# Kernel optimization log

Measured on AMD Instinct MI355X. Metric: run time of the kernel, lower is better.

The kernel has to match this reference:

```python
import jax, jax.numpy as jnp
import numpy as np

N = 100000
E = 1250000
D = 64
R = 16


def _glorot(key, shape):
    fan_in, fan_out = shape[-2], shape[-1]
    lim = jnp.sqrt(6.0 / (fan_in + fan_out))
    return jax.random.uniform(key, shape, jnp.float32, -lim, lim)


def setup_inputs() -> dict:
    key = jax.random.key(0)
    ks = jax.random.split(key, 9)
    x = jax.random.normal(ks[0], (N, D), jnp.float32)
    edge_index = jax.random.randint(ks[1], (2, E), 0, N, jnp.int64 if jax.config.jax_enable_x64 else jnp.int32).astype(jnp.int32)
    edge_type = jax.random.randint(ks[2], (E,), 0, R).astype(jnp.int32)
    return {
        "x": x,
        "edge_index": edge_index,
        "edge_type": edge_type,
        "W1": _glorot(ks[3], (R, D, D)),
        "sw1": _glorot(ks[4], (D, D)),
        "b1": jnp.zeros((D,), jnp.float32),
        "W2": _glorot(ks[5], (R, D, D)),
        "sw2": _glorot(ks[6], (D, D)),
        "b2": jnp.zeros((D,), jnp.float32),
    }


def _rgcn_layer(x, src, dst, edge_type, W, sw, b, residual):
    # self transform [N, O]
    out = x @ sw
    # per-relation transform of all nodes: [N, R, O] (avoids [E, D, O] gathered weights,
    # same math as bmm(x_j, W[edge_type]))
    xW = jnp.einsum('nd,rdo->nro', x, W)
    msg = xW[src, edge_type]                      # [E, O] per-edge messages
    agg = jax.ops.segment_sum(msg, dst, num_segments=N)  # scatter-add aggregate
    out = out + agg
    if residual:
        out = out + x  # Identity residual (in == out channels)
    out = out + b
    return jax.nn.relu(out)


def reference(x, edge_index, edge_type, W1, sw1, b1, W2, sw2, b2):
    src, dst = edge_index[0], edge_index[1]
    # layer 1: residual=True; layer 2: encoding=False -> no residual.
    # activation (relu) applied after every layer by RGCN.forward; dropout p=0 / eval -> no-op.
    h = _rgcn_layer(x, src, dst, edge_type, W1, sw1, b1, residual=True)
    h = _rgcn_layer(h, src, dst, edge_type, W2, sw2, b2, residual=False)
    return h
```

## Files before the change

### kernel.cpp

```cpp
#include <hip/hip_runtime.h>
#include <hip/hip_bf16.h>

#define NN 100000
#define NE 1250000
#define DD 64
#define RR 16
#define NTILE 6250
#define NBINS 100000
#define NBLK_SCAN 391
#define CAPROWS 224
#define DLCAP 576

typedef __attribute__((ext_vector_type(8))) short s16x8;
typedef __attribute__((ext_vector_type(4))) float f32x4;

static __device__ __forceinline__ unsigned short f2bf(float v) {
    __hip_bfloat16 h = __float2bfloat16(v);
    return __builtin_bit_cast(unsigned short, h);
}
static __device__ __forceinline__ unsigned int pack2(float a, float b) {
    return ((unsigned int)f2bf(b) << 16) | (unsigned int)f2bf(a);
}


__global__ void hist_key(const int* __restrict__ dst, const int* __restrict__ et,
                         int* __restrict__ cnt) {
    int e = blockIdx.x * 256 + threadIdx.x;
    if (e < NE) atomicAdd(&cnt[(dst[e] >> 4) * 16 + et[e]], 1);
}

__global__ __launch_bounds__(256) void scan1(const int* __restrict__ cnt,
                                             int* __restrict__ rp, int* __restrict__ part) {
    __shared__ int s[256];
    int i = blockIdx.x * 256 + threadIdx.x;
    int v = (i < NBINS) ? cnt[i] : 0;
    s[threadIdx.x] = v;
    __syncthreads();
    for (int off = 1; off < 256; off <<= 1) {
        int t = (threadIdx.x >= off) ? s[threadIdx.x - off] : 0;
        __syncthreads();
        s[threadIdx.x] += t;
        __syncthreads();
    }
    if (i < NBINS) rp[i] = s[threadIdx.x] - v;
    if (threadIdx.x == 255) part[blockIdx.x] = s[255];
}

__global__ void scan2(int* __restrict__ part, int* __restrict__ rp) {
    __shared__ int s[NBLK_SCAN];
    if (threadIdx.x < NBLK_SCAN) s[threadIdx.x] = part[threadIdx.x];
    __syncthreads();
    if (threadIdx.x == 0) {
        int acc = 0;
        for (int b = 0; b < NBLK_SCAN; ++b) { int t = s[b]; s[b] = acc; acc += t; }
        rp[NBINS] = NE;
    }
    __syncthreads();
    if (threadIdx.x < NBLK_SCAN) part[threadIdx.x] = s[threadIdx.x];
}

__global__ void scan3(int* __restrict__ rp, const int* __restrict__ part, int* __restrict__ cur) {
    int i = blockIdx.x * 256 + threadIdx.x;
    if (i < NBINS) {
        int v = rp[i] + part[blockIdx.x];
        rp[i] = v;
        cur[i] = v;
    }
}

__global__ void scatter_key(const int* __restrict__ src, const int* __restrict__ dst,
                            const int* __restrict__ et, int* __restrict__ cur,
                            unsigned int* __restrict__ ep) {
    int e = blockIdx.x * 256 + threadIdx.x;
    if (e >= NE) return;
    int d = dst[e];
    int p = atomicAdd(&cur[(d >> 4) * 16 + et[e]], 1);
    ep[p] = (unsigned int)src[e] | ((unsigned int)(d & 15) << 20);
}


__global__ void prep_w2(const float* __restrict__ W1, const float* __restrict__ sw1,
                        const float* __restrict__ W2, const float* __restrict__ sw2,
                        unsigned short* __restrict__ wt) {
    int i = blockIdx.x * 256 + threadIdx.x;
    if (i >= 2 * 17 * DD * DD) return;
    int d = i & 63;
    int o = (i >> 6) & 63;
    int p = (i >> 12) % 17;
    int l = i / (17 * DD * DD);
    const float* srcp;
    if (p < 16) srcp = (l ? W2 : W1) + p * DD * DD;
    else        srcp = (l ? sw2 : sw1);
    wt[i] = f2bf(srcp[d * DD + o]);
}

__global__ void prep_x2(const float* __restrict__ x, unsigned short* __restrict__ xb) {
    int i = blockIdx.x * blockDim.x + threadIdx.x;
    if (i < NN * DD) xb[i] = f2bf(x[i]);
}

__global__ __launch_bounds__(256, 5) void fused_layer(
    const unsigned short* __restrict__ xb,
    const unsigned short* __restrict__ wt,
    const int* __restrict__ rp,
    const unsigned int* __restrict__ ep,
    const float* __restrict__ bias,
    const float* __restrict__ xres,
    unsigned short* __restrict__ outb,
    float* __restrict__ outf)
{
    __shared__ __attribute__((aligned(16))) unsigned char Ash[CAPROWS * 128];
    __shared__ __attribute__((aligned(8)))  unsigned char dlb[DLCAP + 32];

    const int tid  = threadIdx.x;
    const int wid  = tid >> 6;
    const int lane = tid & 63;
    const int c = lane & 15;
    const int q = lane >> 4;
    const int tile = blockIdx.x;
    const int n0 = tile * 16;

    const int e0  = rp[tile * 16];
    const int cnt = rp[tile * 16 + 16] - e0;

    {
        const int lim = cnt < DLCAP ? cnt : DLCAP;
        for (int i = tid; i < lim; i += 256)
            dlb[i] = (unsigned char)(ep[e0 + i] >> 20);
        if (tid < 32) {
            int p = lim + tid;
            if (p < DLCAP + 32) dlb[p] = 0xFF;
        }
    }
    {
        const int nrows = cnt < CAPROWS ? cnt : CAPROWS;
        const int half = tid & 1;
        for (int i = tid >> 1; i < nrows; i += 128) {
            int src = (int)(ep[e0 + i] & 0xFFFFF);
            const unsigned short* xr = xb + (size_t)src * DD + half * 32;
            s16x8 v0 = *(const s16x8*)(xr);
            s16x8 v1 = *(const s16x8*)(xr + 8);
            s16x8 v2 = *(const s16x8*)(xr + 16);
            s16x8 v3 = *(const s16x8*)(xr + 24);
            unsigned char* bp = Ash + i * 128;
            const int h8 = (i & 7);
            *(s16x8*)(bp + (((half * 4 + 0) ^ h8) * 16)) = v0;
            *(s16x8*)(bp + (((half * 4 + 1) ^ h8) * 16)) = v1;
            *(s16x8*)(bp + (((half * 4 + 2) ^ h8) * 16)) = v2;
            *(s16x8*)(bp + (((half * 4 + 3) ^ h8) * 16)) = v3;
        }
    }
    __syncthreads();

    const bool dlOK = (cnt <= DLCAP);
    const int och = wid * 16 + c;
    const unsigned short* wbase = wt + (size_t)och * DD + q * 8;
    s16x8 w0 = *(const s16x8*)(wbase);
    s16x8 w1 = *(const s16x8*)(wbase + 32);
    f32x4 Dacc = {0.f, 0.f, 0.f, 0.f};
    const short one = (short)0x3F80;

    for (int r = 0; r < 16; ++r) {
        const unsigned short* nwp = wbase + (size_t)(r + 1) * (DD * DD);
        s16x8 nw0 = *(const s16x8*)(nwp);
        s16x8 nw1 = *(const s16x8*)(nwp + 32);

        const int s0 = rp[tile * 16 + r];
        const int s1 = rp[tile * 16 + r + 1];
        for (int b0 = s0; b0 < s1; b0 += 32) {
            const int rem = s1 - b0;
            const bool hasB = (rem > 16);
            const int lbase = b0 - e0;

            s16x8 a2;
            if (dlOK) {
                const unsigned* dl32 = (const unsigned*)dlb;
                int idx = lbase + q * 4;
                int w = idx >> 2;
                int sh = (idx & 3) * 8;
                unsigned long long pa =
                    ((unsigned long long)dl32[w + 1] << 32) | dl32[w];
                unsigned da = (unsigned)(pa >> sh);
                unsigned db = 0;
                if (hasB) {
                    unsigned long long pb =
                        ((unsigned long long)dl32[w + 5] << 32) | dl32[w + 4];
                    db = (unsigned)(pb >> sh);
                }
                #pragma unroll
                for (int j = 0; j < 4; ++j) {
                    int jj = q * 4 + j;
                    a2[j]     = ((int)((da >> (8 * j)) & 255) == c && jj < rem)
                                ? one : (short)0;
                    a2[j + 4] = (hasB && (int)((db >> (8 * j)) & 255) == c && jj < rem - 16)
                                ? one : (short)0;
                }
            } else {
                int eA = min(b0 + c, s1 - 1);
                unsigned wa = ep[eA];
                int dlA = (b0 + c < s1) ? (int)(wa >> 20) : 31;
                int dlB = 31;
                if (hasB) {
                    int eB = min(b0 + 16 + c, s1 - 1);
                    unsigned wb = ep[eB];
                    dlB = (b0 + 16 + c < s1) ? (int)(wb >> 20) : 31;
                }
                #pragma unroll
                for (int j = 0; j < 4; ++j) {
                    int dj = __shfl(dlA, q * 4 + j, 64);
                    a2[j] = (dj == c) ? one : (short)0;
                    int djb = __shfl(dlB, q * 4 + j, 64);
                    a2[j + 4] = (hasB && djb == c) ? one : (short)0;
                }
            }

            int rA = min(b0 + c, s1 - 1) - e0;
            s16x8 aA0, aA1;
            if (rA < CAPROWS) {
                const unsigned char* ap = Ash + rA * 128;
                const int off = (q ^ (rA & 7)) * 16;
                aA0 = *(const s16x8*)(ap + off);
                aA1 = *(const s16x8*)(ap + (off ^ 64));
            } else {
                int srcA = (int)(ep[e0 + rA] & 0xFFFFF);
                const unsigned short* xr = xb + (size_t)srcA * DD + q * 8;
                aA0 = *(const s16x8*)(xr);
                aA1 = *(const s16x8*)(xr + 32);
            }
            s16x8 aB0, aB1;
            if (hasB) {
                int rB = min(b0 + 16 + c, s1 - 1) - e0;
                if (rB < CAPROWS) {
                    const unsigned char* bp = Ash + rB * 128;
                    const int off = (q ^ (rB & 7)) * 16;
                    aB0 = *(const s16x8*)(bp + off);
                    aB1 = *(const s16x8*)(bp + (off ^ 64));
                } else {
                    int srcB = (int)(ep[e0 + rB] & 0xFFFFF);
                    const unsigned short* xr = xb + (size_t)srcB * DD + q * 8;
                    aB0 = *(const s16x8*)(xr);
                    aB1 = *(const s16x8*)(xr + 32);
                }
            }

            __builtin_amdgcn_s_setprio(1);
            f32x4 cA = {0.f, 0.f, 0.f, 0.f};
            cA = __builtin_amdgcn_mfma_f32_16x16x32_bf16(aA0, w0, cA, 0, 0, 0);
            cA = __builtin_amdgcn_mfma_f32_16x16x32_bf16(aA1, w1, cA, 0, 0, 0);
            s16x8 b2v;
            if (hasB) {
                f32x4 cB = {0.f, 0.f, 0.f, 0.f};
                cB = __builtin_amdgcn_mfma_f32_16x16x32_bf16(aB0, w0, cB, 0, 0, 0);
                cB = __builtin_amdgcn_mfma_f32_16x16x32_bf16(aB1, w1, cB, 0, 0, 0);
                #pragma unroll
                for (int j = 0; j < 4; ++j) {
                    b2v[j]     = (short)f2bf(cA[j]);
                    b2v[j + 4] = (short)f2bf(cB[j]);
                }
            } else {
                #pragma unroll
                for (int j = 0; j < 4; ++j) {
                    b2v[j]     = (short)f2bf(cA[j]);
                    b2v[j + 4] = 0;
                }
            }
            Dacc = __builtin_amdgcn_mfma_f32_16x16x32_bf16(a2, b2v, Dacc, 0, 0, 0);
            __builtin_amdgcn_s_setprio(0);
        }
        w0 = nw0; w1 = nw1;
    }

    {
        const unsigned short* xr = xb + (size_t)(n0 + c) * DD + q * 8;
        s16x8 a0 = *(const s16x8*)(xr);
        s16x8 a1 = *(const s16x8*)(xr + 32);
        Dacc = __builtin_amdgcn_mfma_f32_16x16x32_bf16(a0, w0, Dacc, 0, 0, 0);
        Dacc = __builtin_amdgcn_mfma_f32_16x16x32_bf16(a1, w1, Dacc, 0, 0, 0);
    }

    const float bc = bias[och];
    #pragma unroll
    for (int v = 0; v < 4; ++v) {
        const int node = n0 + q * 4 + v;
        float val = Dacc[v] + bc;
        if (xres) val += xres[(size_t)node * DD + och];
        val = fmaxf(val, 0.f);
        if (outf) outf[(size_t)node * DD + och] = val;
        if (outb) {
            float nb = __shfl_xor(val, 1, 64);
            if (!(c & 1))
                *(unsigned int*)(outb + (size_t)node * DD + och) = pack2(val, nb);
        }
    }
}


extern "C" void kernel_launch(void* const* d_in, const int* in_sizes, int n_in,
                              void* d_out, int out_size, void* d_ws, size_t ws_size,
                              hipStream_t stream)
{
    (void)in_sizes; (void)n_in; (void)out_size; (void)ws_size;
    const float* x    = (const float*)d_in[0];
    const int*   ei   = (const int*)d_in[1];
    const int*   et   = (const int*)d_in[2];
    const float* W1   = (const float*)d_in[3];
    const float* sw1  = (const float*)d_in[4];
    const float* b1   = (const float*)d_in[5];
    const float* W2   = (const float*)d_in[6];
    const float* sw2  = (const float*)d_in[7];
    const float* b2   = (const float*)d_in[8];
    float* out = (float*)d_out;

    const int* srcA = ei;
    const int* dstA = ei + NE;

    char* ws = (char*)d_ws;
    unsigned short* xb   = (unsigned short*)(ws);
    unsigned short* h1b  = (unsigned short*)(ws + 12800000);
    unsigned short* wt2  = (unsigned short*)(ws + 25600000);
    unsigned int*   ep   = (unsigned int*)(ws + 25878528);
    int*            rp   = (int*)(ws + 30878528);
    int*            cnt  = (int*)(ws + 31278544);
    int*            cur  = (int*)(ws + 31678544);
    int*            part = (int*)(ws + 32078544);

    const int NB_E    = (NE + 255) / 256;
    const int NB_ELEM = (NN * DD + 255) / 256;
    const int WPL = 17 * DD * DD;

    hipMemsetAsync(cnt, 0, NBINS * sizeof(int), stream);
    hist_key<<<NB_E, 256, 0, stream>>>(dstA, et, cnt);
    scan1<<<NBLK_SCAN, 256, 0, stream>>>(cnt, rp, part);
    scan2<<<1, 512, 0, stream>>>(part, rp);
    scan3<<<NBLK_SCAN, 256, 0, stream>>>(rp, part, cur);
    scatter_key<<<NB_E, 256, 0, stream>>>(srcA, dstA, et, cur, ep);

    prep_w2<<<(2 * 17 * DD * DD + 255) / 256, 256, 0, stream>>>(W1, sw1, W2, sw2, wt2);
    prep_x2<<<NB_ELEM, 256, 0, stream>>>(x, xb);

    fused_layer<<<NTILE, 256, 0, stream>>>(xb, wt2, rp, ep, b1, x, h1b, nullptr);
    fused_layer<<<NTILE, 256, 0, stream>>>(h1b, wt2 + WPL, rp, ep, b2, nullptr, nullptr, out);
}
```

Baseline: 529.0 us.

## Replace one-hot MFMA aggregation with LDS float atomics and split relations across 8 waves

The fused layer now runs 512 threads per block. Two wave groups each handle 8 relations, with 4 waves per group covering the output channels. Per-edge messages computed by MFMA are accumulated into a shared-memory node-by-channel buffer with workgroup-scope float atomics, replacing the one-hot bf16 MFMA scatter. The epilogue reads the shared buffer with coalesced float2 accesses. This drops the bf16 rounding of messages and the one-hot matrix construction, but it processes 16 edges per step instead of 32 and adds LDS atomic contention plus an extra barrier.

```diff
diff --git a/kernel.cpp b/kernel.cpp
--- a/kernel.cpp
+++ b/kernel.cpp
@@ -10,6 +10,7 @@
 #define NBLK_SCAN 391
 #define CAPROWS 224
 #define DLCAP 576
+#define DNSTRIDE 65
 
 typedef __attribute__((ext_vector_type(8))) short s16x8;
 typedef __attribute__((ext_vector_type(4))) float f32x4;
@@ -20,6 +21,9 @@
 }
 static __device__ __forceinline__ unsigned int pack2(float a, float b) {
     return ((unsigned int)f2bf(b) << 16) | (unsigned int)f2bf(a);
+}
+static __device__ __forceinline__ void lds_addf(float* p, float v) {
+    __hip_atomic_fetch_add(p, v, __ATOMIC_RELAXED, __HIP_MEMORY_SCOPE_WORKGROUP);
 }
 
 
@@ -99,7 +103,7 @@
     if (i < NN * DD) xb[i] = f2bf(x[i]);
 }
 
-__global__ __launch_bounds__(256, 5) void fused_layer(
+__global__ __launch_bounds__(512, 6) void fused_layer(
     const unsigned short* __restrict__ xb,
     const unsigned short* __restrict__ wt,
     const int* __restrict__ rp,
@@ -111,31 +115,34 @@
 {
     __shared__ __attribute__((aligned(16))) unsigned char Ash[CAPROWS * 128];
     __shared__ __attribute__((aligned(8)))  unsigned char dlb[DLCAP + 32];
+    __shared__ __attribute__((aligned(16))) float Dn[16 * DNSTRIDE + 16];
 
     const int tid  = threadIdx.x;
-    const int wid  = tid >> 6;
+    const int w    = tid >> 6;
     const int lane = tid & 63;
     const int c = lane & 15;
     const int q = lane >> 4;
+    const int eh = w >> 2;
+    const int oq = w & 3;
     const int tile = blockIdx.x;
     const int n0 = tile * 16;
 
-    const int e0  = rp[tile * 16];
-    const int cnt = rp[tile * 16 + 16] - e0;
+    int rpv = 0;
+    if (lane < 17) rpv = rp[tile * 16 + lane];
+    const int e0  = __shfl(rpv, 0, 64);
+    const int cnt = __shfl(rpv, 16, 64) - e0;
+
+    for (int i = tid; i < 16 * DNSTRIDE + 16; i += 512) Dn[i] = 0.f;
 
     {
         const int lim = cnt < DLCAP ? cnt : DLCAP;
-        for (int i = tid; i < lim; i += 256)
+        for (int i = tid; i < lim; i += 512)
             dlb[i] = (unsigned char)(ep[e0 + i] >> 20);
-        if (tid < 32) {
-            int p = lim + tid;
-            if (p < DLCAP + 32) dlb[p] = 0xFF;
-        }
     }
     {
         const int nrows = cnt < CAPROWS ? cnt : CAPROWS;
         const int half = tid & 1;
-        for (int i = tid >> 1; i < nrows; i += 128) {
+        for (int i = tid >> 1; i < nrows; i += 256) {
             int src = (int)(ep[e0 + i] & 0xFFFFF);
             const unsigned short* xr = xb + (size_t)src * DD + half * 32;
             s16x8 v0 = *(const s16x8*)(xr);
@@ -153,143 +160,88 @@
     __syncthreads();
 
     const bool dlOK = (cnt <= DLCAP);
-    const int och = wid * 16 + c;
-    const unsigned short* wbase = wt + (size_t)och * DD + q * 8;
-    s16x8 w0 = *(const s16x8*)(wbase);
-    s16x8 w1 = *(const s16x8*)(wbase + 32);
-    f32x4 Dacc = {0.f, 0.f, 0.f, 0.f};
-    const short one = (short)0x3F80;
-
-    for (int r = 0; r < 16; ++r) {
-        const unsigned short* nwp = wbase + (size_t)(r + 1) * (DD * DD);
+    const unsigned short* wb = wt + (size_t)(oq * 16 + c) * DD + q * 8;
+    const int ochBase = oq * 16 + q * 4;
+    const int rbeg = eh * 8;
+
+    s16x8 w0 = *(const s16x8*)(wb + (size_t)rbeg * (DD * DD));
+    s16x8 w1 = *(const s16x8*)(wb + (size_t)rbeg * (DD * DD) + 32);
+
+    for (int r = rbeg; r < rbeg + 8; ++r) {
+        const unsigned short* nwp = wb + (size_t)(r + 1) * (DD * DD);
         s16x8 nw0 = *(const s16x8*)(nwp);
         s16x8 nw1 = *(const s16x8*)(nwp + 32);
 
-        const int s0 = rp[tile * 16 + r];
-        const int s1 = rp[tile * 16 + r + 1];
-        for (int b0 = s0; b0 < s1; b0 += 32) {
-            const int rem = s1 - b0;
-            const bool hasB = (rem > 16);
-            const int lbase = b0 - e0;
-
-            s16x8 a2;
-            if (dlOK) {
-                const unsigned* dl32 = (const unsigned*)dlb;
-                int idx = lbase + q * 4;
-                int w = idx >> 2;
-                int sh = (idx & 3) * 8;
-                unsigned long long pa =
-                    ((unsigned long long)dl32[w + 1] << 32) | dl32[w];
-                unsigned da = (unsigned)(pa >> sh);
-                unsigned db = 0;
-                if (hasB) {
-                    unsigned long long pb =
-                        ((unsigned long long)dl32[w + 5] << 32) | dl32[w + 4];
-                    db = (unsigned)(pb >> sh);
-                }
-                #pragma unroll
-                for (int j = 0; j < 4; ++j) {
-                    int jj = q * 4 + j;
-                    a2[j]     = ((int)((da >> (8 * j)) & 255) == c && jj < rem)
-                                ? one : (short)0;
-                    a2[j + 4] = (hasB && (int)((db >> (8 * j)) & 255) == c && jj < rem - 16)
-                                ? one : (short)0;
-                }
-            } else {
-                int eA = min(b0 + c, s1 - 1);
-                unsigned wa = ep[eA];
-                int dlA = (b0 + c < s1) ? (int)(wa >> 20) : 31;
-                int dlB = 31;
-                if (hasB) {
-                    int eB = min(b0 + 16 + c, s1 - 1);
-                    unsigned wb = ep[eB];
-                    dlB = (b0 + 16 + c < s1) ? (int)(wb >> 20) : 31;
-                }
-                #pragma unroll
-                for (int j = 0; j < 4; ++j) {
-                    int dj = __shfl(dlA, q * 4 + j, 64);
-                    a2[j] = (dj == c) ? one : (short)0;
-                    int djb = __shfl(dlB, q * 4 + j, 64);
-                    a2[j + 4] = (hasB && djb == c) ? one : (short)0;
-                }
-            }
-
-            int rA = min(b0 + c, s1 - 1) - e0;
-            s16x8 aA0, aA1;
+        const int s0 = __shfl(rpv, r, 64);
+        const int s1 = __shfl(rpv, r + 1, 64);
+        for (int b0 = s0; b0 < s1; b0 += 16) {
+            const bool valid = (b0 + c < s1);
+            const int rA = (valid ? b0 + c : s1 - 1) - e0;
+
+            int node;
+            if (dlOK) node = dlb[rA];
+            else      node = (int)(ep[e0 + rA] >> 20);
+
+            s16x8 a0, a1;
             if (rA < CAPROWS) {
                 const unsigned char* ap = Ash + rA * 128;
                 const int off = (q ^ (rA & 7)) * 16;
-                aA0 = *(const s16x8*)(ap + off);
-                aA1 = *(const s16x8*)(ap + (off ^ 64));
+                a0 = *(const s16x8*)(ap + off);
+                a1 = *(const s16x8*)(ap + (off ^ 64));
             } else {
-                int srcA = (int)(ep[e0 + rA] & 0xFFFFF);
-                const unsigned short* xr = xb + (size_t)srcA * DD + q * 8;
-                aA0 = *(const s16x8*)(xr);
-                aA1 = *(const s16x8*)(xr + 32);
+                int src = (int)(ep[e0 + rA] & 0xFFFFF);
+                const unsigned short* xr = xb + (size_t)src * DD + q * 8;
+                a0 = *(const s16x8*)(xr);
+                a1 = *(const s16x8*)(xr + 32);
             }
-            s16x8 aB0, aB1;
-            if (hasB) {
-                int rB = min(b0 + 16 + c, s1 - 1) - e0;
-                if (rB < CAPROWS) {
-                    const unsigned char* bp = Ash + rB * 128;
-                    const int off = (q ^ (rB & 7)) * 16;
-                    aB0 = *(const s16x8*)(bp + off);
-                    aB1 = *(const s16x8*)(bp + (off ^ 64));
-                } else {
-                    int srcB = (int)(ep[e0 + rB] & 0xFFFFF);
-                    const unsigned short* xr = xb + (size_t)srcB * DD + q * 8;
-                    aB0 = *(const s16x8*)(xr);
-                    aB1 = *(const s16x8*)(xr + 32);
-                }
+
+            f32x4 acc = {0.f, 0.f, 0.f, 0.f};
+            acc = __builtin_amdgcn_mfma_f32_16x16x32_bf16(w0, a0, acc, 0, 0, 0);
+            acc = __builtin_amdgcn_mfma_f32_16x16x32_bf16(w1, a1, acc, 0, 0, 0);
+
+            if (valid) {
+                float* dp = Dn + node * DNSTRIDE + ochBase;
+                lds_addf(dp + 0, acc[0]);
+                lds_addf(dp + 1, acc[1]);
+                lds_addf(dp + 2, acc[2]);
+                lds_addf(dp + 3, acc[3]);
             }
-
-            __builtin_amdgcn_s_setprio(1);
-            f32x4 cA = {0.f, 0.f, 0.f, 0.f};
-            cA = __builtin_amdgcn_mfma_f32_16x16x32_bf16(aA0, w0, cA, 0, 0, 0);
-            cA = __builtin_amdgcn_mfma_f32_16x16x32_bf16(aA1, w1, cA, 0, 0, 0);
-            s16x8 b2v;
-            if (hasB) {
-                f32x4 cB = {0.f, 0.f, 0.f, 0.f};
-                cB = __builtin_amdgcn_mfma_f32_16x16x32_bf16(aB0, w0, cB, 0, 0, 0);
-                cB = __builtin_amdgcn_mfma_f32_16x16x32_bf16(aB1, w1, cB, 0, 0, 0);
-                #pragma unroll
-                for (int j = 0; j < 4; ++j) {
-                    b2v[j]     = (short)f2bf(cA[j]);
-                    b2v[j + 4] = (short)f2bf(cB[j]);
-                }
-            } else {
-                #pragma unroll
-                for (int j = 0; j < 4; ++j) {
-                    b2v[j]     = (short)f2bf(cA[j]);
-                    b2v[j + 4] = 0;
-                }
-            }
-            Dacc = __builtin_amdgcn_mfma_f32_16x16x32_bf16(a2, b2v, Dacc, 0, 0, 0);
-            __builtin_amdgcn_s_setprio(0);
         }
         w0 = nw0; w1 = nw1;
     }
 
-    {
+    if (eh) {
         const unsigned short* xr = xb + (size_t)(n0 + c) * DD + q * 8;
         s16x8 a0 = *(const s16x8*)(xr);
         s16x8 a1 = *(const s16x8*)(xr + 32);
-        Dacc = __builtin_amdgcn_mfma_f32_16x16x32_bf16(a0, w0, Dacc, 0, 0, 0);
-        Dacc = __builtin_amdgcn_mfma_f32_16x16x32_bf16(a1, w1, Dacc, 0, 0, 0);
-    }
-
-    const float bc = bias[och];
-    #pragma unroll
-    for (int v = 0; v < 4; ++v) {
-        const int node = n0 + q * 4 + v;
-        float val = Dacc[v] + bc;
-        if (xres) val += xres[(size_t)node * DD + och];
-        val = fmaxf(val, 0.f);
-        if (outf) outf[(size_t)node * DD + och] = val;
-        if (outb) {
-            float nb = __shfl_xor(val, 1, 64);
-            if (!(c & 1))
-                *(unsigned int*)(outb + (size_t)node * DD + och) = pack2(val, nb);
+        f32x4 acc = {0.f, 0.f, 0.f, 0.f};
+        acc = __builtin_amdgcn_mfma_f32_16x16x32_bf16(w0, a0, acc, 0, 0, 0);
+        acc = __builtin_amdgcn_mfma_f32_16x16x32_bf16(w1, a1, acc, 0, 0, 0);
+        float* dp = Dn + c * DNSTRIDE + ochBase;
+        lds_addf(dp + 0, acc[0]);
+        lds_addf(dp + 1, acc[1]);
+        lds_addf(dp + 2, acc[2]);
+        lds_addf(dp + 3, acc[3]);
+    }
+    __syncthreads();
+
+    {
+        const int idx  = tid * 2;
+        const int node = idx >> 6;
+        const int och  = idx & 63;
+        float v0 = Dn[node * DNSTRIDE + och]     + bias[och];
+        float v1 = Dn[node * DNSTRIDE + och + 1] + bias[och + 1];
+        if (xres) {
+            const float2 rv = *(const float2*)(xres + (size_t)(n0 + node) * DD + och);
+            v0 += rv.x; v1 += rv.y;
+        }
+        v0 = fmaxf(v0, 0.f);
+        v1 = fmaxf(v1, 0.f);
+        if (outb)
+            *(unsigned int*)(outb + (size_t)(n0 + node) * DD + och) = pack2(v0, v1);
+        if (outf) {
+            float2 o = {v0, v1};
+            *(float2*)(outf + (size_t)(n0 + node) * DD + och) = o;
         }
     }
 }
@@ -338,6 +290,6 @@
     prep_w2<<<(2 * 17 * DD * DD + 255) / 256, 256, 0, stream>>>(W1, sw1, W2, sw2, wt2);
     prep_x2<<<NB_ELEM, 256, 0, stream>>>(x, xb);
 
-    fused_layer<<<NTILE, 256, 0, stream>>>(xb, wt2, rp, ep, b1, x, h1b, nullptr);
-    fused_layer<<<NTILE, 256, 0, stream>>>(h1b, wt2 + WPL, rp, ep, b2, nullptr, nullptr, out);
-}
+    fused_layer<<<NTILE, 512, 0, stream>>>(xb, wt2, rp, ep, b1, x, h1b, nullptr);
+    fused_layer<<<NTILE, 512, 0, stream>>>(h1b, wt2 + WPL, rp, ep, b2, nullptr, nullptr, out);
+}
```

Result: slower. 1.200 ms (+126.9%).

## Process 16 edges per step with dual accumulators and shuffled row pointers

Applied to the files above, without the earlier changes.

Restructures the per-relation edge loop to handle 16 edges per iteration instead of 32, and alternates two relation planes into two independent accumulators so the dependent MFMA chains can overlap. Row-pointer values are loaded once per wave and broadcast with shuffles instead of repeated global loads. Launch bounds are relaxed from 5 to 4 blocks per CU to give the compiler more registers. The cost is more loop iterations per relation, half-empty MFMA operands in the aggregation step, and possibly lower occupancy.

```diff
diff --git a/kernel.cpp b/kernel.cpp
--- a/kernel.cpp
+++ b/kernel.cpp
@@ -99,7 +99,7 @@
     if (i < NN * DD) xb[i] = f2bf(x[i]);
 }
 
-__global__ __launch_bounds__(256, 5) void fused_layer(
+__global__ __launch_bounds__(256, 4) void fused_layer(
     const unsigned short* __restrict__ xb,
     const unsigned short* __restrict__ wt,
     const int* __restrict__ rp,
@@ -120,8 +120,10 @@
     const int tile = blockIdx.x;
     const int n0 = tile * 16;
 
-    const int e0  = rp[tile * 16];
-    const int cnt = rp[tile * 16 + 16] - e0;
+    int rpv = 0;
+    if (lane < 17) rpv = rp[tile * 16 + lane];
+    const int e0  = __shfl(rpv, 0, 64);
+    const int cnt = __shfl(rpv, 16, 64) - e0;
 
     {
         const int lim = cnt < DLCAP ? cnt : DLCAP;
@@ -155,24 +157,16 @@
     const bool dlOK = (cnt <= DLCAP);
     const int och = wid * 16 + c;
     const unsigned short* wbase = wt + (size_t)och * DD + q * 8;
-    s16x8 w0 = *(const s16x8*)(wbase);
-    s16x8 w1 = *(const s16x8*)(wbase + 32);
-    f32x4 Dacc = {0.f, 0.f, 0.f, 0.f};
     const short one = (short)0x3F80;
 
-    for (int r = 0; r < 16; ++r) {
-        const unsigned short* nwp = wbase + (size_t)(r + 1) * (DD * DD);
-        s16x8 nw0 = *(const s16x8*)(nwp);
-        s16x8 nw1 = *(const s16x8*)(nwp + 32);
-
-        const int s0 = rp[tile * 16 + r];
-        const int s1 = rp[tile * 16 + r + 1];
-        for (int b0 = s0; b0 < s1; b0 += 32) {
+    auto plane_body = [&](int r, s16x8 W0, s16x8 W1, f32x4& Dst) {
+        const int s0 = __shfl(rpv, r, 64);
+        const int s1 = __shfl(rpv, r + 1, 64);
+        for (int b0 = s0; b0 < s1; b0 += 16) {
             const int rem = s1 - b0;
-            const bool hasB = (rem > 16);
             const int lbase = b0 - e0;
 
-            s16x8 a2;
+            unsigned da;
             if (dlOK) {
                 const unsigned* dl32 = (const unsigned*)dlb;
                 int idx = lbase + q * 4;
@@ -180,103 +174,81 @@
                 int sh = (idx & 3) * 8;
                 unsigned long long pa =
                     ((unsigned long long)dl32[w + 1] << 32) | dl32[w];
-                unsigned da = (unsigned)(pa >> sh);
-                unsigned db = 0;
-                if (hasB) {
-                    unsigned long long pb =
-                        ((unsigned long long)dl32[w + 5] << 32) | dl32[w + 4];
-                    db = (unsigned)(pb >> sh);
-                }
-                #pragma unroll
-                for (int j = 0; j < 4; ++j) {
-                    int jj = q * 4 + j;
-                    a2[j]     = ((int)((da >> (8 * j)) & 255) == c && jj < rem)
-                                ? one : (short)0;
-                    a2[j + 4] = (hasB && (int)((db >> (8 * j)) & 255) == c && jj < rem - 16)
-                                ? one : (short)0;
-                }
+                da = (unsigned)(pa >> sh);
             } else {
                 int eA = min(b0 + c, s1 - 1);
                 unsigned wa = ep[eA];
-                int dlA = (b0 + c < s1) ? (int)(wa >> 20) : 31;
-                int dlB = 31;
-                if (hasB) {
-                    int eB = min(b0 + 16 + c, s1 - 1);
-                    unsigned wb = ep[eB];
-                    dlB = (b0 + 16 + c < s1) ? (int)(wb >> 20) : 31;
-                }
-                #pragma unroll
-                for (int j = 0; j < 4; ++j) {
-                    int dj = __shfl(dlA, q * 4 + j, 64);
-                    a2[j] = (dj == c) ? one : (short)0;
-                    int djb = __shfl(dlB, q * 4 + j, 64);
-                    a2[j + 4] = (hasB && djb == c) ? one : (short)0;
-                }
+                int dl = (b0 + c < s1) ? (int)(wa >> 20) : 31;
+                unsigned x0 = (unsigned)__shfl(dl, q * 4 + 0, 64) & 255u;
+                unsigned x1 = (unsigned)__shfl(dl, q * 4 + 1, 64) & 255u;
+                unsigned x2 = (unsigned)__shfl(dl, q * 4 + 2, 64) & 255u;
+                unsigned x3 = (unsigned)__shfl(dl, q * 4 + 3, 64) & 255u;
+                da = x0 | (x1 << 8) | (x2 << 16) | (x3 << 24);
             }
+            s16x8 a2;
+            #pragma unroll
+            for (int j = 0; j < 4; ++j) {
+                int jj = q * 4 + j;
+                a2[j] = ((int)((da >> (8 * j)) & 255) == c && jj < rem) ? one : (short)0;
+                a2[j + 4] = 0;
+            }
 
             int rA = min(b0 + c, s1 - 1) - e0;
-            s16x8 aA0, aA1;
+            s16x8 a0, a1;
             if (rA < CAPROWS) {
                 const unsigned char* ap = Ash + rA * 128;
                 const int off = (q ^ (rA & 7)) * 16;
-                aA0 = *(const s16x8*)(ap + off);
-                aA1 = *(const s16x8*)(ap + (off ^ 64));
+                a0 = *(const s16x8*)(ap + off);
+                a1 = *(const s16x8*)(ap + (off ^ 64));
             } else {
-                int srcA = (int)(ep[e0 + rA] & 0xFFFFF);
-                const unsigned short* xr = xb + (size_t)srcA * DD + q * 8;
-                aA0 = *(const s16x8*)(xr);
-                aA1 = *(const s16x8*)(xr + 32);
-            }
-            s16x8 aB0, aB1;
-            if (hasB) {
-                int rB = min(b0 + 16 + c, s1 - 1) - e0;
-                if (rB < CAPROWS) {
-                    const unsigned char* bp = Ash + rB * 128;
-                    const int off = (q ^ (rB & 7)) * 16;
-                    aB0 = *(const s16x8*)(bp + off);
-                    aB1 = *(const s16x8*)(bp + (off ^ 64));
-                } else {
-                    int srcB = (int)(ep[e0 + rB] & 0xFFFFF);
-                    const unsigned short* xr = xb + (size_t)srcB * DD + q * 8;
-                    aB0 = *(const s16x8*)(xr);
-                    aB1 = *(const s16x8*)(xr + 32);
-                }
+                int src = (int)(ep[e0 + rA] & 0xFFFFF);
+                const unsigned short* xr = xb + (size_t)src * DD + q * 8;
+                a0 = *(const s16x8*)(xr);
+                a1 = *(const s16x8*)(xr + 32);
             }
 
             __builtin_amdgcn_s_setprio(1);
             f32x4 cA = {0.f, 0.f, 0.f, 0.f};
-            cA = __builtin_amdgcn_mfma_f32_16x16x32_bf16(aA0, w0, cA, 0, 0, 0);
-            cA = __builtin_amdgcn_mfma_f32_16x16x32_bf16(aA1, w1, cA, 0, 0, 0);
-            s16x8 b2v;
-            if (hasB) {
-                f32x4 cB = {0.f, 0.f, 0.f, 0.f};
-                cB = __builtin_amdgcn_mfma_f32_16x16x32_bf16(aB0, w0, cB, 0, 0, 0);
-                cB = __builtin_amdgcn_mfma_f32_16x16x32_bf16(aB1, w1, cB, 0, 0, 0);
-                #pragma unroll
-                for (int j = 0; j < 4; ++j) {
-                    b2v[j]     = (short)f2bf(cA[j]);
-                    b2v[j + 4] = (short)f2bf(cB[j]);
-                }
-            } else {
-                #pragma unroll
-                for (int j = 0; j < 4; ++j) {
-                    b2v[j]     = (short)f2bf(cA[j]);
-                    b2v[j + 4] = 0;
-                }
+            cA = __builtin_amdgcn_mfma_f32_16x16x32_bf16(a0, W0, cA, 0, 0, 0);
+            cA = __builtin_amdgcn_mfma_f32_16x16x32_bf16(a1, W1, cA, 0, 0, 0);
+            s16x8 bv;
+            #pragma unroll
+            for (int j = 0; j < 4; ++j) {
+                bv[j]     = (short)f2bf(cA[j]);
+                bv[j + 4] = 0;
             }
-            Dacc = __builtin_amdgcn_mfma_f32_16x16x32_bf16(a2, b2v, Dacc, 0, 0, 0);
+            Dst = __builtin_amdgcn_mfma_f32_16x16x32_bf16(a2, bv, Dst, 0, 0, 0);
             __builtin_amdgcn_s_setprio(0);
         }
-        w0 = nw0; w1 = nw1;
+    };
+
+    s16x8 wc0 = *(const s16x8*)(wbase);
+    s16x8 wc1 = *(const s16x8*)(wbase + 32);
+    f32x4 D0 = {0.f, 0.f, 0.f, 0.f};
+    f32x4 D1 = {0.f, 0.f, 0.f, 0.f};
+
+    for (int rr = 0; rr < 8; ++rr) {
+        const int r = rr * 2;
+        const unsigned short* p1 = wbase + (size_t)(r + 1) * (DD * DD);
+        s16x8 wn0 = *(const s16x8*)(p1);
+        s16x8 wn1 = *(const s16x8*)(p1 + 32);
+        plane_body(r, wc0, wc1, D0);
+        const int r2 = (r + 2 <= 16) ? r + 2 : 16;
+        const unsigned short* p2 = wbase + (size_t)r2 * (DD * DD);
+        s16x8 t0 = *(const s16x8*)(p2);
+        s16x8 t1 = *(const s16x8*)(p2 + 32);
+        plane_body(r + 1, wn0, wn1, D1);
+        wc0 = t0; wc1 = t1;
     }
 
     {
         const unsigned short* xr = xb + (size_t)(n0 + c) * DD + q * 8;
         s16x8 a0 = *(const s16x8*)(xr);
         s16x8 a1 = *(const s16x8*)(xr + 32);
-        Dacc = __builtin_amdgcn_mfma_f32_16x16x32_bf16(a0, w0, Dacc, 0, 0, 0);
-        Dacc = __builtin_amdgcn_mfma_f32_16x16x32_bf16(a1, w1, Dacc, 0, 0, 0);
-    }
+        D0 = __builtin_amdgcn_mfma_f32_16x16x32_bf16(a0, wc0, D0, 0, 0, 0);
+        D1 = __builtin_amdgcn_mfma_f32_16x16x32_bf16(a1, wc1, D1, 0, 0, 0);
+    }
+    f32x4 Dacc = D0 + D1;
 
     const float bc = bias[och];
     #pragma unroll
```

New measurement: 527.2 us. No clear change (-0.3%).
